# Kernel optimization log

Measured on AMD Instinct MI355X. Metric: run time of the kernel, lower is better.

## Reference

```python
import jax, jax.numpy as jnp
import numpy as np

EMBED_DIM = 512
NUM_HEADS = 8
HEAD_DIM = EMBED_DIM // NUM_HEADS
SCALING = HEAD_DIM ** -0.5
T, B = 2048, 4
NEG_INF = -1e9


def setup_inputs() -> dict:
    key = jax.random.key(0)
    k1, k2, k3 = jax.random.split(key, 3)
    h = jax.random.normal(k1, (T, B, EMBED_DIM), dtype=jnp.float32)
    # causal additive mask, [T, T]: 0 on/below diagonal, -inf above
    attn_mask = jnp.where(jnp.triu(jnp.ones((T, T), dtype=bool), k=1), NEG_INF, 0.0).astype(jnp.float32)
    in_proj_weight = jax.random.normal(k2, (3 * EMBED_DIM, EMBED_DIM), dtype=jnp.float32) * 0.02
    in_proj_bias = jnp.zeros((3 * EMBED_DIM,), dtype=jnp.float32)
    out_w = jax.random.normal(k3, (EMBED_DIM, EMBED_DIM), dtype=jnp.float32) * 0.02
    out_b = jnp.zeros((EMBED_DIM,), dtype=jnp.float32)
    return {"h": h, "attn_mask": attn_mask, "in_proj_weight": in_proj_weight,
            "in_proj_bias": in_proj_bias, "out_w": out_w, "out_b": out_b}


def reference(h, attn_mask, in_proj_weight, in_proj_bias, out_w, out_b):
    tgt_len, bsz, embed_dim = h.shape
    # fused QKV projection: [T, B, 3E]
    qkv = jnp.einsum('tbe,fe->tbf', h, in_proj_weight) + in_proj_bias
    q, k, v = jnp.split(qkv, 3, axis=-1)
    q = q * SCALING
    # [T, B, E] -> [B*H, T, hd]
    def to_heads(x):
        return x.reshape(tgt_len, bsz * NUM_HEADS, HEAD_DIM).transpose(1, 0, 2)
    q, k, v = to_heads(q), to_heads(k), to_heads(v)
    # scores: [B*H, T, S]
    attn_weights = jnp.einsum('bth,bsh->bts', q, k)
    attn_weights = attn_weights + attn_mask[None, :, :]
    attn_p = jax.nn.softmax(attn_weights, axis=-1)
    attn = jnp.einsum('bts,bsh->bth', attn_p, v)
    # [B*H, T, hd] -> [T, B, E]
    attn = attn.transpose(1, 0, 2).reshape(tgt_len, bsz, embed_dim)
    out = jnp.einsum('tbe,fe->tbf', attn, out_w) + out_b
    return out, attn_p.reshape(bsz, NUM_HEADS, tgt_len, tgt_len)
```

## Files before the change

### kernel.cpp

```cpp
#include <hip/hip_runtime.h>
#include <cstdint>
#include <cstddef>

#define T_SEQ 2048
#define BSZ 4
#define EMB 512
#define NH 8
#define HD 64
#define SCALING 0.125f
#define NEGBIG (-1e30f)
#define PW 144

typedef short bf16x8_t __attribute__((ext_vector_type(8)));
typedef float f32x4_t __attribute__((ext_vector_type(4)));
typedef short short4v __attribute__((ext_vector_type(4)));
typedef float float4v __attribute__((ext_vector_type(4)));

typedef __attribute__((address_space(1))) const void* as1_cvp;
typedef __attribute__((address_space(3))) void* as3_vp;

#define MFMA16(a, b, c) __builtin_amdgcn_mfma_f32_16x16x32_bf16((a), (b), (c), 0, 0, 0)

static __device__ __forceinline__ short f2b(float f) {
  union { float f; uint32_t u; } x; x.f = f;
  uint32_t r = (x.u + 0x7fffu + ((x.u >> 16) & 1u)) >> 16;
  return (short)(r & 0xffffu);
}

static __device__ __forceinline__ void gload_lds16(const void* g, void* l) {
  __builtin_amdgcn_global_load_lds((as1_cvp)g, (as3_vp)l, 16, 0, 0);
}

__global__ __launch_bounds__(256) void cvt_kernel(const float* __restrict__ in,
                                                  short* __restrict__ out) {
  int i = (blockIdx.x * 256 + threadIdx.x) * 4;
  float4v v = *(const float4v*)(in + i);
  short4v o;
  o[0] = f2b(v[0]); o[1] = f2b(v[1]); o[2] = f2b(v[2]); o[3] = f2b(v[3]);
  *(short4v*)(out + i) = o;
}

template <int EPI>
__global__ __launch_bounds__(256)
void gemm_bt(const short* __restrict__ A, const short* __restrict__ Bt,
             const float* __restrict__ bias,
             short* __restrict__ outQ, short* __restrict__ outK, short* __restrict__ outV,
             float* __restrict__ outF) {
  __shared__ short ldsA[128 * 32];
  __shared__ short ldsB[128 * 32];
  const int tid = threadIdx.x;
  const int wid = tid >> 6, lane = tid & 63, g = lane >> 4, r16 = lane & 15;
  const int wr = wid >> 1, wc = wid & 1;
  const int mbase = blockIdx.y * 128, nbase = blockIdx.x * 128;

  f32x4_t acc[4][4];
#pragma unroll
  for (int m = 0; m < 4; ++m)
#pragma unroll
    for (int n = 0; n < 4; ++n) acc[m][n] = (f32x4_t){0.f, 0.f, 0.f, 0.f};

  for (int kt = 0; kt < 16; ++kt) {
    __syncthreads();
#pragma unroll
    for (int i = 0; i < 2; ++i) {
      int c = i * 256 + tid;
      int row = c >> 2, j4 = c & 3;
      gload_lds16(A + (size_t)(mbase + row) * 512 + kt * 32 + j4 * 8, &ldsA[c * 8]);
      gload_lds16(Bt + (size_t)(nbase + row) * 512 + kt * 32 + j4 * 8, &ldsB[c * 8]);
    }
    __syncthreads();
    bf16x8_t af[4], bfv[4];
#pragma unroll
    for (int m = 0; m < 4; ++m)
      af[m] = *(const bf16x8_t*)&ldsA[(wr * 64 + m * 16 + r16) * 32 + g * 8];
#pragma unroll
    for (int n = 0; n < 4; ++n)
      bfv[n] = *(const bf16x8_t*)&ldsB[(wc * 64 + n * 16 + r16) * 32 + g * 8];
#pragma unroll
    for (int m = 0; m < 4; ++m)
#pragma unroll
      for (int n = 0; n < 4; ++n) acc[m][n] = MFMA16(af[m], bfv[n], acc[m][n]);
  }

#pragma unroll
  for (int m = 0; m < 4; ++m) {
#pragma unroll
    for (int n = 0; n < 4; ++n) {
      int col = nbase + wc * 64 + n * 16 + r16;
      float bcol = bias[col];
#pragma unroll
      for (int j = 0; j < 4; ++j) {
        int row = mbase + wr * 64 + m * 16 + g * 4 + j;
        float v = acc[m][n][j] + bcol;
        if (EPI == 0) {
          int sect = col >> 9, e = col & 511, hh = e >> 6, d = e & 63;
          int t = row >> 2, b = row & 3;
          size_t dst = ((size_t)(b * NH + hh) * T_SEQ + t) * HD + d;
          short bv = f2b(v);
          if (sect == 0) outQ[dst] = bv;
          else if (sect == 1) outK[dst] = bv;
          else outV[dst] = bv;
        } else {
          outF[(size_t)row * EMB + col] = v;
        }
      }
    }
  }
}

__global__ __launch_bounds__(256)
void attn_fused(const short* __restrict__ Qg, const short* __restrict__ Kg,
                const short* __restrict__ Vg, float* __restrict__ Pout,
                short* __restrict__ attnO) {
  __shared__ __align__(16) short lds[26624];
  short* Kt = lds;
  short* Vt = lds + 8192;
  short(*Pl)[16 * PW] = (short(*)[16 * PW])(lds + 8192 + 9216);
  const int bh = blockIdx.x;
  const int qt = 31 - (int)blockIdx.y;
  const int tid = threadIdx.x, wid = tid >> 6, lane = tid & 63;
  const int g = lane >> 4, r16 = lane & 15;
  const size_t headOff = (size_t)bh * T_SEQ * HD;
  const int wrow0 = qt * 64 + wid * 16;
  const int myrow = wrow0 + r16;
  const int maxcol = qt * 64 + 64;
  const int nt128 = (qt >> 1) + 1;
  const short* Kh = Kg + headOff;
  const short* Vh = Vg + headOff;

  bf16x8_t qf[2];
  {
    const short* qp = Qg + headOff + (size_t)myrow * HD + g * 8;
    qf[0] = *(const bf16x8_t*)qp;
    qf[1] = *(const bf16x8_t*)(qp + 32);
  }

  float m_w = NEGBIG;
  float l_w = 0.f;
  f32x4_t oacc[4];
#pragma unroll
  for (int dc = 0; dc < 4; ++dc) oacc[dc] = (f32x4_t){0.f, 0.f, 0.f, 0.f};

  uint32_t* Vtu = (uint32_t*)Vt;
  const int kp0 = tid & 63, dg0 = tid >> 6;

  bf16x8_t va[2], vb[2];
#define VLOAD(KB)                                                              \
  {                                                                            \
    const short* vp0 = Vh + (size_t)((KB) + kp0 * 2) * HD + dg0 * 8;           \
    va[0] = *(const bf16x8_t*)vp0; vb[0] = *(const bf16x8_t*)(vp0 + HD);       \
    const short* vp1 = vp0 + 32;                                               \
    va[1] = *(const bf16x8_t*)vp1; vb[1] = *(const bf16x8_t*)(vp1 + HD);       \
  }
  VLOAD(0)

  for (int kt = 0; kt < nt128; ++kt) {
    const int kb = kt * 128;
    __syncthreads();
#pragma unroll
    for (int i = 0; i < 4; ++i) {
      int cc = i * 256 + tid;
      int row = cc >> 3, j8 = (cc & 7) ^ (row & 7);
      gload_lds16(Kh + (size_t)(kb + row) * HD + j8 * 8, &Kt[cc * 8]);
    }
#pragma unroll
    for (int i = 0; i < 2; ++i) {
      int dg = dg0 + i * 4;
#pragma unroll
      for (int j = 0; j < 8; ++j)
        Vtu[(dg * 8 + j) * (PW / 2) + kp0] =
            (uint32_t)(uint16_t)va[i][j] | ((uint32_t)(uint16_t)vb[i][j] << 16);
    }
    __syncthreads();
    if (kt + 1 < nt128) VLOAD(kb + 128)
    const int H = ((maxcol - kb) >= 128) ? 2 : 1;
#pragma unroll
    for (int h = 0; h < 2; ++h) {
      if (h < H) {
        float sv[4][4];
#pragma unroll
        for (int kc4 = 0; kc4 < 4; ++kc4) {
          const int rl = (h * 4 + kc4) * 16 + r16;
          f32x4_t s = {0.f, 0.f, 0.f, 0.f};
#pragma unroll
          for (int kk = 0; kk < 2; ++kk) {
            int byteo = (rl * 128 + kk * 64 + g * 16) ^ ((rl & 7) << 4);
            bf16x8_t kf = *(const bf16x8_t*)((const char*)Kt + byteo);
            s = MFMA16(kf, qf[kk], s);
          }
          const int key0 = kb + (h * 4 + kc4) * 16 + g * 4;
#pragma unroll
          for (int j = 0; j < 4; ++j)
            sv[kc4][j] = (key0 + j <= myrow) ? s[j] * SCALING : NEGBIG;
        }
        float pm = NEGBIG;
#pragma unroll
        for (int kc4 = 0; kc4 < 4; ++kc4)
#pragma unroll
          for (int j = 0; j < 4; ++j) pm = fmaxf(pm, sv[kc4][j]);
#pragma unroll
        for (int off = 1; off < 64; off <<= 1) pm = fmaxf(pm, __shfl_xor(pm, off));
        float mn = fmaxf(m_w, pm);
        if (mn > m_w + 8.f) {
          float sc = __expf(m_w - mn);
          l_w *= sc;
#pragma unroll
          for (int dc = 0; dc < 4; ++dc)
#pragma unroll
            for (int j = 0; j < 4; ++j) oacc[dc][j] *= sc;
          m_w = mn;
        }
#pragma unroll
        for (int kc4 = 0; kc4 < 4; ++kc4) {
          short4v pb;
#pragma unroll
          for (int j = 0; j < 4; ++j) {
            float e = __expf(sv[kc4][j] - m_w);
            l_w += e;
            pb[j] = f2b(e);
          }
          *(short4v*)&Pl[wid][r16 * PW + (h * 4 + kc4) * 16 + g * 4] = pb;
        }
#pragma unroll
        for (int kk2 = 0; kk2 < 2; ++kk2) {
          const int kc2 = h * 2 + kk2;
          bf16x8_t pf = *(const bf16x8_t*)&Pl[wid][r16 * PW + kc2 * 32 + g * 8];
#pragma unroll
          for (int dc = 0; dc < 4; ++dc) {
            bf16x8_t vf = *(const bf16x8_t*)&Vt[(dc * 16 + r16) * PW + kc2 * 32 + g * 8];
            oacc[dc] = MFMA16(pf, vf, oacc[dc]);
          }
        }
      }
    }
  }

#pragma unroll
  for (int off = 16; off <= 32; off <<= 1) l_w += __shfl_xor(l_w, off);
  const float rl2 = 1.0f / l_w;

  float lo[4];
#pragma unroll
  for (int j = 0; j < 4; ++j) lo[j] = 1.0f / __shfl(l_w, g * 4 + j);
#pragma unroll
  for (int dc = 0; dc < 4; ++dc) {
#pragma unroll
    for (int j = 0; j < 4; ++j) {
      int t = wrow0 + g * 4 + j, d = dc * 16 + r16;
      size_t ntok = (size_t)t * BSZ + (bh >> 3);
      attnO[ntok * EMB + (bh & 7) * HD + d] = f2b(oacc[dc][j] * lo[j]);
    }
  }

  short* Kb0 = lds;
  short* Kb1 = lds + 8192;
  float* Prow = Pout + ((size_t)bh * T_SEQ + myrow) * T_SEQ;

#define STAGEK(KB, BUF)                                                        \
  {                                                                            \
    _Pragma("unroll")                                                          \
    for (int i = 0; i < 4; ++i) {                                              \
      int cc = i * 256 + tid;                                                  \
      int row = cc >> 3, j8 = (cc & 7) ^ (row & 7);                            \
      gload_lds16(Kh + (size_t)((KB) + row) * HD + j8 * 8, &(BUF)[cc * 8]);    \
    }                                                                          \
  }

  __syncthreads();
  STAGEK(0, Kb0)
  __syncthreads();
  int p = 0;
  for (int kt = 0; kt < nt128; ++kt) {
    const int kb = kt * 128;
    short* cur = p ? Kb1 : Kb0;
    short* nxt = p ? Kb0 : Kb1;
    const bool more = (kt + 1 < nt128);
    if (more) {
      STAGEK(kb + 128, nxt)
      __builtin_amdgcn_sched_barrier(0);
    }
    const int navail = (maxcol - kb) >> 4;
    const int nkc = navail < 8 ? navail : 8;
#pragma unroll
    for (int kc = 0; kc < 8; ++kc) {
      if (kc < nkc) {
        const int rl = kc * 16 + r16;
        f32x4_t s = {0.f, 0.f, 0.f, 0.f};
#pragma unroll
        for (int kk = 0; kk < 2; ++kk) {
          int byteo = (rl * 128 + kk * 64 + g * 16) ^ ((rl & 7) << 4);
          bf16x8_t kf = *(const bf16x8_t*)((const char*)cur + byteo);
          s = MFMA16(kf, qf[kk], s);
        }
        const int key0 = kb + kc * 16 + g * 4;
        float4v pvv;
#pragma unroll
        for (int j = 0; j < 4; ++j) {
          float e = __expf(s[j] * SCALING - m_w) * rl2;
          pvv[j] = (key0 + j <= myrow) ? e : 0.f;
        }
        *(float4v*)(Prow + key0) = pvv;
      }
    }
    if (more) {
      __builtin_amdgcn_sched_barrier(0);
      asm volatile("s_waitcnt vmcnt(8)" ::: "memory");
      __builtin_amdgcn_s_barrier();
      __builtin_amdgcn_sched_barrier(0);
    }
    p ^= 1;
  }

  const int c0 = maxcol;
  const int nc4 = (T_SEQ - c0) >> 2;
  for (int r = 0; r < 64; ++r) {
    size_t base = ((size_t)bh * T_SEQ + qt * 64 + r) * T_SEQ + c0;
    for (int c4 = tid; c4 < nc4; c4 += 256) {
      float4v z = {0.f, 0.f, 0.f, 0.f};
      *(float4v*)(Pout + base + (size_t)c4 * 4) = z;
    }
  }
}

extern "C" void kernel_launch(void* const* d_in, const int* in_sizes, int n_in,
                              void* d_out, int out_size, void* d_ws, size_t ws_size,
                              hipStream_t stream) {
  const float* h = (const float*)d_in[0];
  const float* w_in = (const float*)d_in[2];
  const float* b_in = (const float*)d_in[3];
  const float* w_out = (const float*)d_in[4];
  const float* b_out = (const float*)d_in[5];
  float* out = (float*)d_out;
  float* Pout = out + (size_t)T_SEQ * BSZ * EMB;

  short* hB = (short*)d_ws;
  short* wB = hB + (size_t)8192 * 512;
  short* owB = wB + (size_t)1536 * 512;
  short* qB = owB + (size_t)512 * 512;
  short* kB = qB + (size_t)32 * 2048 * 64;
  short* vB = kB + (size_t)32 * 2048 * 64;
  short* aB = vB + (size_t)32 * 2048 * 64;

  cvt_kernel<<<4096, 256, 0, stream>>>(h, hB);
  cvt_kernel<<<768, 256, 0, stream>>>(w_in, wB);
  cvt_kernel<<<256, 256, 0, stream>>>(w_out, owB);

  gemm_bt<0><<<dim3(12, 64), 256, 0, stream>>>(hB, wB, b_in, qB, kB, vB, nullptr);
  attn_fused<<<dim3(32, 32), 256, 0, stream>>>(qB, kB, vB, Pout, aB);
  gemm_bt<1><<<dim3(4, 64), 256, 0, stream>>>(aB, owB, b_out, nullptr, nullptr, nullptr, out);
}
```

Baseline: 222.8 us.

## Restructure attention first pass into double-buffered 64-key tiles with async K prefetch

The first (output-accumulation) pass now walks keys in 64-wide tiles instead of 128-wide, double-buffering K in LDS and prefetching the next K tile and V registers while the current tile computes. Manual waitcnt and s_barrier replace the two __syncthreads per tile, and a per-chunk check skips causal masking for fully unmasked chunks. LDS shrinks from about 52KB to 34KB, which may allow more blocks per CU. In exchange there are twice as many loop iterations and barriers, and the hand-counted vmcnt values are fragile if the load count changes.

Result: no change. 225.1 us (+1.1%).

```diff
diff --git a/kernel.cpp b/kernel.cpp
--- a/kernel.cpp
+++ b/kernel.cpp
@@ -9,7 +9,7 @@
 #define HD 64
 #define SCALING 0.125f
 #define NEGBIG (-1e30f)
-#define PW 144
+#define PW 72
 
 typedef short bf16x8_t __attribute__((ext_vector_type(8)));
 typedef float f32x4_t __attribute__((ext_vector_type(4)));
@@ -112,10 +112,11 @@
 void attn_fused(const short* __restrict__ Qg, const short* __restrict__ Kg,
                 const short* __restrict__ Vg, float* __restrict__ Pout,
                 short* __restrict__ attnO) {
-  __shared__ __align__(16) short lds[26624];
-  short* Kt = lds;
+  __shared__ __align__(16) short lds[17408];
+  short* Kb0 = lds;
+  short* Kb1 = lds + 4096;
   short* Vt = lds + 8192;
-  short(*Pl)[16 * PW] = (short(*)[16 * PW])(lds + 8192 + 9216);
+  short(*Pl)[16 * PW] = (short(*)[16 * PW])(lds + 12800);
   const int bh = blockIdx.x;
   const int qt = 31 - (int)blockIdx.y;
   const int tid = threadIdx.x, wid = tid >> 6, lane = tid & 63;
@@ -124,6 +125,7 @@
   const int wrow0 = qt * 64 + wid * 16;
   const int myrow = wrow0 + r16;
   const int maxcol = qt * 64 + 64;
+  const int nt64 = qt + 1;
   const int nt128 = (qt >> 1) + 1;
   const short* Kh = Kg + headOff;
   const short* Vh = Vg + headOff;
@@ -142,96 +144,111 @@
   for (int dc = 0; dc < 4; ++dc) oacc[dc] = (f32x4_t){0.f, 0.f, 0.f, 0.f};
 
   uint32_t* Vtu = (uint32_t*)Vt;
-  const int kp0 = tid & 63, dg0 = tid >> 6;
-
-  bf16x8_t va[2], vb[2];
-#define VLOAD(KB)                                                              \
+  const int kp0 = tid & 31, dg0 = tid >> 5;
+
+  bf16x8_t va, vb;
+#define VLOAD64(KB)                                                            \
   {                                                                            \
     const short* vp0 = Vh + (size_t)((KB) + kp0 * 2) * HD + dg0 * 8;           \
-    va[0] = *(const bf16x8_t*)vp0; vb[0] = *(const bf16x8_t*)(vp0 + HD);       \
-    const short* vp1 = vp0 + 32;                                               \
-    va[1] = *(const bf16x8_t*)vp1; vb[1] = *(const bf16x8_t*)(vp1 + HD);       \
-  }
-  VLOAD(0)
-
-  for (int kt = 0; kt < nt128; ++kt) {
-    const int kb = kt * 128;
-    __syncthreads();
-#pragma unroll
-    for (int i = 0; i < 4; ++i) {
-      int cc = i * 256 + tid;
-      int row = cc >> 3, j8 = (cc & 7) ^ (row & 7);
-      gload_lds16(Kh + (size_t)(kb + row) * HD + j8 * 8, &Kt[cc * 8]);
-    }
-#pragma unroll
-    for (int i = 0; i < 2; ++i) {
-      int dg = dg0 + i * 4;
-#pragma unroll
-      for (int j = 0; j < 8; ++j)
-        Vtu[(dg * 8 + j) * (PW / 2) + kp0] =
-            (uint32_t)(uint16_t)va[i][j] | ((uint32_t)(uint16_t)vb[i][j] << 16);
-    }
-    __syncthreads();
-    if (kt + 1 < nt128) VLOAD(kb + 128)
-    const int H = ((maxcol - kb) >= 128) ? 2 : 1;
-#pragma unroll
-    for (int h = 0; h < 2; ++h) {
-      if (h < H) {
-        float sv[4][4];
-#pragma unroll
-        for (int kc4 = 0; kc4 < 4; ++kc4) {
-          const int rl = (h * 4 + kc4) * 16 + r16;
-          f32x4_t s = {0.f, 0.f, 0.f, 0.f};
-#pragma unroll
-          for (int kk = 0; kk < 2; ++kk) {
-            int byteo = (rl * 128 + kk * 64 + g * 16) ^ ((rl & 7) << 4);
-            bf16x8_t kf = *(const bf16x8_t*)((const char*)Kt + byteo);
-            s = MFMA16(kf, qf[kk], s);
-          }
-          const int key0 = kb + (h * 4 + kc4) * 16 + g * 4;
-#pragma unroll
-          for (int j = 0; j < 4; ++j)
-            sv[kc4][j] = (key0 + j <= myrow) ? s[j] * SCALING : NEGBIG;
-        }
-        float pm = NEGBIG;
-#pragma unroll
-        for (int kc4 = 0; kc4 < 4; ++kc4)
-#pragma unroll
-          for (int j = 0; j < 4; ++j) pm = fmaxf(pm, sv[kc4][j]);
-#pragma unroll
-        for (int off = 1; off < 64; off <<= 1) pm = fmaxf(pm, __shfl_xor(pm, off));
-        float mn = fmaxf(m_w, pm);
-        if (mn > m_w + 8.f) {
-          float sc = __expf(m_w - mn);
-          l_w *= sc;
-#pragma unroll
-          for (int dc = 0; dc < 4; ++dc)
-#pragma unroll
-            for (int j = 0; j < 4; ++j) oacc[dc][j] *= sc;
-          m_w = mn;
-        }
-#pragma unroll
-        for (int kc4 = 0; kc4 < 4; ++kc4) {
-          short4v pb;
-#pragma unroll
-          for (int j = 0; j < 4; ++j) {
-            float e = __expf(sv[kc4][j] - m_w);
-            l_w += e;
-            pb[j] = f2b(e);
-          }
-          *(short4v*)&Pl[wid][r16 * PW + (h * 4 + kc4) * 16 + g * 4] = pb;
-        }
-#pragma unroll
-        for (int kk2 = 0; kk2 < 2; ++kk2) {
-          const int kc2 = h * 2 + kk2;
-          bf16x8_t pf = *(const bf16x8_t*)&Pl[wid][r16 * PW + kc2 * 32 + g * 8];
-#pragma unroll
-          for (int dc = 0; dc < 4; ++dc) {
-            bf16x8_t vf = *(const bf16x8_t*)&Vt[(dc * 16 + r16) * PW + kc2 * 32 + g * 8];
-            oacc[dc] = MFMA16(pf, vf, oacc[dc]);
-          }
-        }
-      }
+    va = *(const bf16x8_t*)vp0;                                                \
+    vb = *(const bf16x8_t*)(vp0 + HD);                                         \
+  }
+#define STAGEK64(KB, BUF)                                                      \
+  {                                                                            \
+    _Pragma("unroll")                                                          \
+    for (int i = 0; i < 2; ++i) {                                              \
+      int cc = i * 256 + tid;                                                  \
+      int row = cc >> 3, j8 = (cc & 7) ^ (row & 7);                            \
+      gload_lds16(Kh + (size_t)((KB) + row) * HD + j8 * 8, &(BUF)[cc * 8]);    \
+    }                                                                          \
+  }
+
+  VLOAD64(0)
+  STAGEK64(0, Kb0)
+
+  for (int kt = 0; kt < nt64; ++kt) {
+    const int kb = kt * 64;
+    short* Kcur = (kt & 1) ? Kb1 : Kb0;
+    short* Knxt = (kt & 1) ? Kb0 : Kb1;
+    const bool more = (kt + 1 < nt64);
+#pragma unroll
+    for (int j = 0; j < 8; ++j)
+      Vtu[(dg0 * 8 + j) * (PW / 2) + kp0] =
+          (uint32_t)(uint16_t)va[j] | ((uint32_t)(uint16_t)vb[j] << 16);
+    if (more) {
+      STAGEK64(kb + 64, Knxt)
+      VLOAD64(kb + 64)
+    }
+    __builtin_amdgcn_sched_barrier(0);
+    if (kt == 0) {
+      if (more) asm volatile("s_waitcnt vmcnt(4) lgkmcnt(0)" ::: "memory");
+      else      asm volatile("s_waitcnt vmcnt(0) lgkmcnt(0)" ::: "memory");
+    } else {
+      asm volatile("s_waitcnt lgkmcnt(0)" ::: "memory");
+    }
+    __builtin_amdgcn_s_barrier();
+    __builtin_amdgcn_sched_barrier(0);
+
+    float sv[4][4];
+#pragma unroll
+    for (int kc4 = 0; kc4 < 4; ++kc4) {
+      const int rl = kc4 * 16 + r16;
+      f32x4_t s = {0.f, 0.f, 0.f, 0.f};
+#pragma unroll
+      for (int kk = 0; kk < 2; ++kk) {
+        int byteo = (rl * 128 + kk * 64 + g * 16) ^ ((rl & 7) << 4);
+        bf16x8_t kf = *(const bf16x8_t*)((const char*)Kcur + byteo);
+        s = MFMA16(kf, qf[kk], s);
+      }
+      const int key0 = kb + kc4 * 16 + g * 4;
+      const bool nomask = (kb + kc4 * 16 + 15 <= wrow0);
+#pragma unroll
+      for (int j = 0; j < 4; ++j)
+        sv[kc4][j] = (nomask || key0 + j <= myrow) ? s[j] * SCALING : NEGBIG;
+    }
+    float pm = NEGBIG;
+#pragma unroll
+    for (int kc4 = 0; kc4 < 4; ++kc4)
+#pragma unroll
+      for (int j = 0; j < 4; ++j) pm = fmaxf(pm, sv[kc4][j]);
+#pragma unroll
+    for (int off = 1; off < 64; off <<= 1) pm = fmaxf(pm, __shfl_xor(pm, off));
+    float mn = fmaxf(m_w, pm);
+    if (mn > m_w + 8.f) {
+      float sc = __expf(m_w - mn);
+      l_w *= sc;
+#pragma unroll
+      for (int dc = 0; dc < 4; ++dc)
+#pragma unroll
+        for (int j = 0; j < 4; ++j) oacc[dc][j] *= sc;
+      m_w = mn;
+    }
+#pragma unroll
+    for (int kc4 = 0; kc4 < 4; ++kc4) {
+      short4v pb;
+#pragma unroll
+      for (int j = 0; j < 4; ++j) {
+        float e = __expf(sv[kc4][j] - m_w);
+        l_w += e;
+        pb[j] = f2b(e);
+      }
+      *(short4v*)&Pl[wid][r16 * PW + kc4 * 16 + g * 4] = pb;
+    }
+#pragma unroll
+    for (int kc2 = 0; kc2 < 2; ++kc2) {
+      bf16x8_t pf = *(const bf16x8_t*)&Pl[wid][r16 * PW + kc2 * 32 + g * 8];
+#pragma unroll
+      for (int dc = 0; dc < 4; ++dc) {
+        bf16x8_t vf = *(const bf16x8_t*)&Vt[(dc * 16 + r16) * PW + kc2 * 32 + g * 8];
+        oacc[dc] = MFMA16(pf, vf, oacc[dc]);
+      }
+    }
+
+    if (more) {
+      __builtin_amdgcn_sched_barrier(0);
+      asm volatile("s_waitcnt vmcnt(2)" ::: "memory");
+      __builtin_amdgcn_s_barrier();
+      __builtin_amdgcn_sched_barrier(0);
     }
   }
 
@@ -252,11 +269,11 @@
     }
   }
 
-  short* Kb0 = lds;
-  short* Kb1 = lds + 8192;
+  short* K2b0 = lds;
+  short* K2b1 = lds + 8192;
   float* Prow = Pout + ((size_t)bh * T_SEQ + myrow) * T_SEQ;
 
-#define STAGEK(KB, BUF)                                                        \
+#define STAGEK128(KB, BUF)                                                     \
   {                                                                            \
     _Pragma("unroll")                                                          \
     for (int i = 0; i < 4; ++i) {                                              \
@@ -267,16 +284,16 @@
   }
 
   __syncthreads();
-  STAGEK(0, Kb0)
+  STAGEK128(0, K2b0)
   __syncthreads();
   int p = 0;
   for (int kt = 0; kt < nt128; ++kt) {
     const int kb = kt * 128;
-    short* cur = p ? Kb1 : Kb0;
-    short* nxt = p ? Kb0 : Kb1;
+    short* cur = p ? K2b1 : K2b0;
+    short* nxt = p ? K2b0 : K2b1;
     const bool more = (kt + 1 < nt128);
     if (more) {
-      STAGEK(kb + 128, nxt)
+      STAGEK128(kb + 128, nxt)
       __builtin_amdgcn_sched_barrier(0);
     }
     const int navail = (maxcol - kb) >> 4;
```
